# Kernel tuning notes

Measured on AMD Instinct MI355X. Metric: run time of the kernel, lower is better.

## Reference

```python
import jax, jax.numpy as jnp
import numpy as np

B, D, H, K, N = 1024, 768, 8, 10, 50000
LN_EPS = 1e-5


def _ln(x, g, b):
    m = x.mean(-1, keepdims=True)
    v = ((x - m) ** 2).mean(-1, keepdims=True)
    return (x - m) * jax.lax.rsqrt(v + LN_EPS) * g + b


def _normalize(x):
    n = jnp.sqrt(jnp.sum(x * x, -1, keepdims=True))
    return x / jnp.maximum(n, 1e-12)


def _mha(q, k, v, in_w, in_b, out_w, out_b, h=H):
    # torch nn.MultiheadAttention (batch_first, eval): packed in_proj then out_proj
    d = q.shape[-1]
    dh = d // h
    wq, wk, wv = jnp.split(in_w, 3, axis=0)
    bq, bk, bv = jnp.split(in_b, 3, axis=0)
    def proj(x, w, b):
        bsz, s, _ = x.shape
        return (x @ w.T + b).reshape(bsz, s, h, dh)
    qh, kh, vh = proj(q, wq, bq), proj(k, wk, bk), proj(v, wv, bv)
    att = jnp.einsum('bqhd,bkhd->bhqk', qh, kh) * (1.0 / np.sqrt(dh))
    att = jax.nn.softmax(att, axis=-1)
    o = jnp.einsum('bhqk,bkhd->bqhd', att, vh).reshape(q.shape[0], q.shape[1], d)
    return o @ out_w.T + out_b


def setup_inputs() -> dict:
    key = jax.random.key(0)
    ks = iter(jax.random.split(key, 32))
    s = 0.05
    r = lambda shp, sc=s: jax.random.normal(next(ks), shp, jnp.float32) * sc
    return {
        'visual_feat': r((B, D), 1.0), 'text_feat': r((B, D), 1.0),
        'ans_emb': r((N, D), 1.0),
        'vqa_in_w': r((3 * D, D)), 'vqa_in_b': jnp.zeros((3 * D,)),
        'vqa_out_w': r((D, D)), 'vqa_out_b': jnp.zeros((D,)),
        'fproj_w': r((D, 2 * D)), 'fproj_b': jnp.zeros((D,)),
        'fln_g': jnp.ones((D,)), 'fln_b': jnp.zeros((D,)),
        'sim_w': r((D, D)), 'sim_b': jnp.zeros((D,)),
        'mha_in_w': r((5, 3 * D, D)), 'mha_in_b': jnp.zeros((5, 3 * D)),
        'mha_out_w': r((5, D, D)), 'mha_out_b': jnp.zeros((5, D)),
        'ffn_w1': r((4 * D, D)), 'ffn_b1': jnp.zeros((4 * D,)),
        'ffn_w2': r((D, 4 * D)), 'ffn_b2': jnp.zeros((D,)),
        'ln_g': jnp.ones((4, D)), 'ln_b': jnp.zeros((4, D)),
        'outp_w': r((D, D)), 'outp_b': jnp.zeros((D,)),
        'open_w1': r((D, D)), 'open_b1': jnp.zeros((D,)),
        'open_w2': r((N, D)), 'open_b2': jnp.zeros((N,)),
    }


def reference(visual_feat, text_feat, ans_emb, vqa_in_w, vqa_in_b, vqa_out_w,
              vqa_out_b, fproj_w, fproj_b, fln_g, fln_b, sim_w, sim_b,
              mha_in_w, mha_in_b, mha_out_w, mha_out_b, ffn_w1, ffn_b1,
              ffn_w2, ffn_b2, ln_g, ln_b, outp_w, outp_b, open_w1, open_b1,
              open_w2, open_b2):
    gelu = lambda x: jax.nn.gelu(x, approximate=False)
    vis = visual_feat[:, None, :]   # [B,1,D]
    txt = text_feat[:, None, :]

    # --- SemanticAnswerDistillation ---
    attn_q = _mha(txt, vis, vis, vqa_in_w, vqa_in_b, vqa_out_w, vqa_out_b)[:, 0]
    fused = jnp.concatenate([visual_feat, attn_q], -1) @ fproj_w.T + fproj_b
    fused = gelu(_ln(fused, fln_g, fln_b))
    fused_proj = fused @ sim_w.T + sim_b
    sim = _normalize(fused_proj) @ _normalize(ans_emb).T   # [B,N] cosine sim
    topk_scores, topk_idx = jax.lax.top_k(sim, K)
    topk_emb = ans_emb[topk_idx]                           # [B,K,D] gather

    # --- CrossModalFusion --- (MHA order: vs, ts, v2t, t2v, ans)
    m = lambda i, q, k, v: _mha(q, k, v, mha_in_w[i], mha_in_b[i], mha_out_w[i], mha_out_b[i])
    v1 = _ln(vis + m(0, vis, vis, vis), ln_g[0], ln_b[0])
    t1 = _ln(txt + m(1, txt, txt, txt), ln_g[1], ln_b[1])
    fz = _ln(m(2, v1, t1, t1) + m(3, t1, v1, v1), ln_g[2], ln_b[2])
    ag = m(4, fz, topk_emb, topk_emb)
    fz = _ln(fz + ag, ln_g[3], ln_b[3])
    fz = fz + (gelu(fz @ ffn_w1.T + ffn_b1) @ ffn_w2.T + ffn_b2)
    out = fz[:, 0] @ outp_w.T + outp_b                     # [B,D]

    # --- open head ---
    open_logits = gelu(out @ open_w1.T + open_b1) @ open_w2.T + open_b2
    return open_logits
```

## Files before the change

### kernel.cpp

```cpp
#include <hip/hip_runtime.h>
#include <hip/hip_bf16.h>

#define D_  768
#define B_  1024
#define N_  50000
#define K_  10
#define CH2_ 12500
#define NCH2_ 4
#define CM2_ 16
#define KPT_ 49

__device__ __forceinline__ float gelu_f(float x){ return 0.5f*x*(1.0f+erff(x*0.70710678118654752f)); }
__device__ __forceinline__ double gelu_d(double x){ return 0.5*x*(1.0+erf(x*0.707106781186547524400844362105)); }

__device__ __forceinline__ float block_sum(float v, float* sm){
  #pragma unroll
  for (int o=32;o>0;o>>=1) v += __shfl_xor(v,o);
  __syncthreads();
  if ((threadIdx.x&63)==0) sm[threadIdx.x>>6]=v;
  __syncthreads();
  return (sm[0]+sm[1])+(sm[2]+sm[3]);
}
__device__ __forceinline__ double block_sum64(double v, double* sm){
  #pragma unroll
  for (int o=32;o>0;o>>=1) v += __shfl_xor(v,o);
  __syncthreads();
  if ((threadIdx.x&63)==0) sm[threadIdx.x>>6]=v;
  __syncthreads();
  return (sm[0]+sm[1])+(sm[2]+sm[3]);
}

template<int ASRC, int EPI>
__global__ __launch_bounds__(256)
void dgemm_k(const void* __restrict__ Ap, const float* __restrict__ Wp, size_t woff,
             const float* __restrict__ biasp, size_t boff, double* __restrict__ Cp,
             int M, int N, int Kd, int ldc)
{
  __shared__ double As[16][64];
  __shared__ double Bs[16][64];
  const int t  = threadIdx.x;
  const int tx = t & 15, ty = t >> 4;
  const int row0 = blockIdx.y << 6, col0 = blockIdx.x << 6;
  const int lr = t >> 2, lk = (t & 3) << 2;
  const int ar = row0 + lr;
  const int wn = col0 + lr;
  const float* Wf = Wp + woff;
  double acc[4][4] = {};
  for (int k0 = 0; k0 < Kd; k0 += 16) {
    double av[4], wv[4];
    if (ar < M) {
      if (ASRC==0){
        const double* a = (const double*)Ap + (size_t)ar*Kd + k0 + lk;
        av[0]=a[0]; av[1]=a[1]; av[2]=a[2]; av[3]=a[3];
      } else {
        float4 v = *(const float4*)((const float*)Ap + (size_t)ar*Kd + k0 + lk);
        av[0]=(double)v.x; av[1]=(double)v.y; av[2]=(double)v.z; av[3]=(double)v.w;
      }
    } else { av[0]=av[1]=av[2]=av[3]=0.0; }
    if (wn < N) {
      float4 v = *(const float4*)(Wf + (size_t)wn*Kd + k0 + lk);
      wv[0]=(double)v.x; wv[1]=(double)v.y; wv[2]=(double)v.z; wv[3]=(double)v.w;
    } else { wv[0]=wv[1]=wv[2]=wv[3]=0.0; }
    #pragma unroll
    for (int u=0;u<4;++u){ As[lk+u][lr]=av[u]; Bs[lk+u][lr]=wv[u]; }
    __syncthreads();
    #pragma unroll
    for (int kk=0;kk<16;++kk){
      double aa[4], bb[4];
      #pragma unroll
      for (int u=0;u<4;++u){ aa[u]=As[kk][(ty<<2)+u]; bb[u]=Bs[kk][(tx<<2)+u]; }
      #pragma unroll
      for (int i=0;i<4;++i)
        #pragma unroll
        for (int j=0;j<4;++j)
          acc[i][j] = fma(aa[i], bb[j], acc[i][j]);
    }
    __syncthreads();
  }
  #pragma unroll
  for (int i=0;i<4;++i){
    int r=row0+(ty<<2)+i; if (r>=M) continue;
    #pragma unroll
    for (int j=0;j<4;++j){
      int n=col0+(tx<<2)+j; if (n>=N) continue;
      double v=acc[i][j];
      if (EPI) v += (double)(biasp+boff)[n];
      Cp[(size_t)r*ldc+n]=v;
    }
  }
}

__global__ __launch_bounds__(256)
void ln64_k(const double* __restrict__ x0, const float* __restrict__ g,
            const float* __restrict__ b, double* __restrict__ y)
{
  __shared__ double sm[4];
  size_t base = (size_t)blockIdx.x * D_;
  double xv[3]; double s=0.0;
  #pragma unroll
  for (int i=0;i<3;++i){ int c=threadIdx.x+(i<<8); xv[i]=x0[base+c]; s+=xv[i]; }
  s = block_sum64(s, sm);
  double m = s*(1.0/768.0);
  double vs=0.0;
  #pragma unroll
  for (int i=0;i<3;++i){ double d=xv[i]-m; vs+=d*d; }
  vs = block_sum64(vs, sm);
  double inv = 1.0/sqrt(vs*(1.0/768.0)+1e-5);
  #pragma unroll
  for (int i=0;i<3;++i){
    int c=threadIdx.x+(i<<8);
    double o=(xv[i]-m)*inv*(double)g[c]+(double)b[c];
    y[base+c]=gelu_d(o);
  }
}

template<int SRC>
__global__ __launch_bounds__(256)
void rnorm64w_k(const void* __restrict__ x, double* __restrict__ invn, int M)
{
  int gw = (blockIdx.x*256 + threadIdx.x) >> 6;
  int lane = threadIdx.x & 63;
  if (gw >= M) return;
  size_t base = (size_t)gw * D_;
  double s = 0.0;
  #pragma unroll
  for (int k=0;k<12;++k){
    double v = (SRC==1) ? (double)((const float*)x)[base+lane+(k<<6)]
                        : ((const double*)x)[base+lane+(k<<6)];
    s = fma(v,v,s);
  }
  #pragma unroll
  for (int o=32;o>0;o>>=1) s += __shfl_xor(s,o);
  if (lane==0) invn[gw] = 1.0/fmax(sqrt(s),1e-12);
}

__global__ void d2f_k(const double* __restrict__ src, float* __restrict__ dst, int n)
{ int i=blockIdx.x*256+threadIdx.x; if (i<n) dst[i]=(float)src[i]; }

__global__ void prep64_k(const float* __restrict__ vis, double* __restrict__ fusedin)
{
  int i = blockIdx.x*256+threadIdx.x;
  if (i >= B_*D_) return;
  int r=i/D_, c=i-r*D_;
  fusedin[(size_t)r*(2*D_)+c]=(double)vis[i];
}

template<int EPI, int SCALE>
__global__ __launch_bounds__(256)
void gemm128_k(const float* __restrict__ Ap, const float* __restrict__ Wp,
               const float* __restrict__ biasp, float* __restrict__ Cp,
               const float* __restrict__ inva, const float* __restrict__ invw,
               int M, int N, int Kd, int ldc)
{
  __shared__ __align__(16) float As[16][128];
  __shared__ __align__(16) float Bs[16][128];
  const int t = threadIdx.x;
  const int tx = t & 15, ty = t >> 4;
  const int row0 = blockIdx.y << 7, col0 = blockIdx.x << 7;
  const int lr = t >> 1, lk8 = (t & 1) << 3;
  const int arow = row0 + lr;
  const int wrow = col0 + lr;
  float acc[8][8] = {};
  for (int k0 = 0; k0 < Kd; k0 += 16){
    float4 a0 = *(const float4*)(Ap + (size_t)arow*Kd + k0 + lk8);
    float4 a1 = *(const float4*)(Ap + (size_t)arow*Kd + k0 + lk8 + 4);
    float4 b0 = {0,0,0,0}, b1 = {0,0,0,0};
    if (wrow < N){
      b0 = *(const float4*)(Wp + (size_t)wrow*Kd + k0 + lk8);
      b1 = *(const float4*)(Wp + (size_t)wrow*Kd + k0 + lk8 + 4);
    }
    As[lk8+0][lr]=a0.x; As[lk8+1][lr]=a0.y; As[lk8+2][lr]=a0.z; As[lk8+3][lr]=a0.w;
    As[lk8+4][lr]=a1.x; As[lk8+5][lr]=a1.y; As[lk8+6][lr]=a1.z; As[lk8+7][lr]=a1.w;
    Bs[lk8+0][lr]=b0.x; Bs[lk8+1][lr]=b0.y; Bs[lk8+2][lr]=b0.z; Bs[lk8+3][lr]=b0.w;
    Bs[lk8+4][lr]=b1.x; Bs[lk8+5][lr]=b1.y; Bs[lk8+6][lr]=b1.z; Bs[lk8+7][lr]=b1.w;
    __syncthreads();
    #pragma unroll
    for (int kk=0; kk<16; ++kk){
      float4 aL = *(const float4*)&As[kk][ty<<2];
      float4 aH = *(const float4*)&As[kk][64 + (ty<<2)];
      float4 bL = *(const float4*)&Bs[kk][tx<<2];
      float4 bH = *(const float4*)&Bs[kk][64 + (tx<<2)];
      float av[8] = {aL.x,aL.y,aL.z,aL.w, aH.x,aH.y,aH.z,aH.w};
      float bv[8] = {bL.x,bL.y,bL.z,bL.w, bH.x,bH.y,bH.z,bH.w};
      #pragma unroll
      for (int i=0;i<8;++i)
        #pragma unroll
        for (int j=0;j<8;++j)
          acc[i][j] = fmaf(av[i], bv[j], acc[i][j]);
    }
    __syncthreads();
  }
  #pragma unroll
  for (int i=0;i<8;++i){
    int r = row0 + ((i<4) ? ((ty<<2)+i) : (64 + (ty<<2) + i - 4));
    float ia = SCALE ? inva[r] : 1.f;
    #pragma unroll
    for (int jh=0;jh<2;++jh){
      int cbase = col0 + ((jh==0) ? (tx<<2) : (64 + (tx<<2)));
      #pragma unroll
      for (int j=0;j<4;++j){
        int c = cbase + j;
        if (c >= N) continue;
        float v = acc[i][jh*4+j];
        if (EPI) v += biasp[c];
        if (SCALE) v = v * ia * invw[c];
        Cp[(size_t)r*ldc + c] = v;
      }
    }
  }
}

template<int ATY, int EPI, int SCALE>
__global__ __launch_bounds__(256)
void gemm_k(const float* __restrict__ Ap, const int* __restrict__ ridx,
            const float* __restrict__ Wp, size_t woff,
            const float* __restrict__ biasp, size_t boff, float* __restrict__ Cp,
            const float* __restrict__ inva32, const float* __restrict__ invw32,
            int M, int N, int Kd, int ldc)
{
  __shared__ __align__(16) float As[16][64];
  __shared__ __align__(16) float Bs[16][64];
  const int t  = threadIdx.x;
  const int tx = t & 15, ty = t >> 4;
  const int row0 = blockIdx.y << 6, col0 = blockIdx.x << 6;
  const int lr = t >> 2, lk = (t & 3) << 2;
  const int ar = row0 + lr;
  const int wn = col0 + lr;
  const float* Wf = Wp + woff;
  float acc[4][4] = {};
  int arow = ar;
  if (ATY==3 && ar < M){
    arow = ridx[ar];
    if ((unsigned)arow >= (unsigned)N_) arow = 0;
  }
  for (int k0 = 0; k0 < Kd; k0 += 16) {
    float av[4], wv[4];
    if (ar < M) {
      float4 v = *(const float4*)(Ap + (size_t)arow*Kd + k0 + lk);
      av[0]=v.x; av[1]=v.y; av[2]=v.z; av[3]=v.w;
    } else { av[0]=av[1]=av[2]=av[3]=0.f; }
    if (wn < N) {
      float4 v = *(const float4*)(Wf + (size_t)wn*Kd + k0 + lk);
      wv[0]=v.x; wv[1]=v.y; wv[2]=v.z; wv[3]=v.w;
    } else { wv[0]=wv[1]=wv[2]=wv[3]=0.f; }
    #pragma unroll
    for (int u=0;u<4;++u){ As[lk+u][lr]=av[u]; Bs[lk+u][lr]=wv[u]; }
    __syncthreads();
    #pragma unroll
    for (int kk=0;kk<16;++kk){
      float4 a4 = *(const float4*)&As[kk][ty<<2];
      float4 b4 = *(const float4*)&Bs[kk][tx<<2];
      float aa[4]={a4.x,a4.y,a4.z,a4.w};
      float bb[4]={b4.x,b4.y,b4.z,b4.w};
      #pragma unroll
      for (int i=0;i<4;++i)
        #pragma unroll
        for (int j=0;j<4;++j)
          acc[i][j] = fmaf(aa[i], bb[j], acc[i][j]);
    }
    __syncthreads();
  }
  float bv[4];
  #pragma unroll
  for (int j=0;j<4;++j){
    int n=col0+(tx<<2)+j;
    bv[j] = (EPI>=1 && n<N) ? (biasp+boff)[n] : 0.f;
  }
  #pragma unroll
  for (int i=0;i<4;++i){
    int r=row0+(ty<<2)+i; if (r>=M) continue;
    float ia = (SCALE && r<M) ? inva32[r] : 1.f;
    #pragma unroll
    for (int j=0;j<4;++j){
      int n=col0+(tx<<2)+j; if (n>=N) continue;
      float v=acc[i][j]+bv[j];
      if (EPI==2) v=gelu_f(v);
      if (SCALE) v = v * ia * invw32[n];
      Cp[(size_t)r*ldc+n]=v;
    }
  }
}

template<int RES>
__global__ __launch_bounds__(256)
void ln_k(const float* __restrict__ x0, const float* __restrict__ resf,
          const float* __restrict__ resb,
          const float* __restrict__ g, const float* __restrict__ b, size_t gboff,
          float* __restrict__ y)
{
  __shared__ float sm[4];
  size_t base = (size_t)blockIdx.x * D_;
  float xv[3]; float s=0.f;
  #pragma unroll
  for (int i=0;i<3;++i){
    int c=threadIdx.x+(i<<8);
    float tv=x0[base+c];
    if (RES==1) tv+=resf[base+c];
    if (RES==2) tv+=resb[base+c];
    xv[i]=tv; s+=tv;
  }
  s = block_sum(s, sm);
  float m = s*(1.0f/768.0f);
  float vs=0.f;
  #pragma unroll
  for (int i=0;i<3;++i){ float d=xv[i]-m; vs+=d*d; }
  vs = block_sum(vs, sm);
  float inv = rsqrtf(vs*(1.0f/768.0f)+1e-5f);
  #pragma unroll
  for (int i=0;i<3;++i){
    int c=threadIdx.x+(i<<8);
    y[base+c]=(xv[i]-m)*inv*(g+gboff)[c]+(b+gboff)[c];
  }
}

__global__ void add_k(const float* __restrict__ a, const float* __restrict__ b, float* __restrict__ c, int n)
{ int i=blockIdx.x*256+threadIdx.x; if (i<n) c[i]=a[i]+b[i]; }

__global__ __launch_bounds__(256)
void topk16_chunk_k(const float* __restrict__ simc, int* __restrict__ cand_id,
                    int off, int chunk, int cn, int ldc)
{
  __shared__ float rs[4];
  __shared__ int   ri[4];
  __shared__ float bs_s;
  __shared__ int   bi_s;
  int b = blockIdx.x, t = threadIdx.x;
  const float* rowp = simc + (size_t)b*ldc;
  float v[KPT_];
  #pragma unroll
  for (int k=0;k<KPT_;++k){
    int j = t + (k<<8);
    v[k] = (j < cn) ? rowp[j] : -1e30f;
  }
  float ps = 1e30f; int pi = -1;
  for (int round=0; round<CM2_; ++round){
    float ms = -1e30f; int mi = 0x7fffffff;
    #pragma unroll
    for (int k=0;k<KPT_;++k){
      int j = t + (k<<8);
      float s = v[k];
      bool elig = (s < ps) || (s == ps && j > pi);
      if (elig && (s > ms || (s == ms && j < mi))){ ms = s; mi = j; }
    }
    #pragma unroll
    for (int o=32;o>0;o>>=1){
      float os = __shfl_xor(ms, o); int oi = __shfl_xor(mi, o);
      if (os > ms || (os == ms && oi < mi)){ ms = os; mi = oi; }
    }
    if ((t&63)==0){ rs[t>>6]=ms; ri[t>>6]=mi; }
    __syncthreads();
    if (t==0){
      float gs=rs[0]; int gi=ri[0];
      #pragma unroll
      for (int w=1;w<4;++w) if (rs[w]>gs || (rs[w]==gs && ri[w]<gi)){ gs=rs[w]; gi=ri[w]; }
      bs_s=gs; bi_s=gi;
      cand_id[((size_t)b*NCH2_+chunk)*CM2_+round] = (gi==0x7fffffff) ? 0x7fffffff : off+gi;
    }
    __syncthreads();
    ps = bs_s; pi = bi_s;
  }
}

__global__ __launch_bounds__(256)
void rescore_k(const double* __restrict__ fproj64, const float* __restrict__ ans,
               const int* __restrict__ cand_id,
               const double* __restrict__ inv_fp64, const double* __restrict__ inv_an64,
               int* __restrict__ run_id)
{
  __shared__ double q[D_];
  __shared__ double sc_s[NCH2_*CM2_];
  __shared__ int    id_s[NCH2_*CM2_];
  int b = blockIdx.x, t = threadIdx.x;
  int wave = t>>6, lane = t&63;
  for (int i=t;i<D_;i+=256) q[i]=fproj64[(size_t)b*D_+i];
  __syncthreads();
  for (int c = wave; c < NCH2_*CM2_; c += 4){
    int j = cand_id[(size_t)b*NCH2_*CM2_ + c];
    bool ok = ((unsigned)j < (unsigned)N_);
    double acc = 0.0;
    if (ok){
      const float* ar = ans + (size_t)j*D_;
      #pragma unroll
      for (int k=0;k<12;++k){
        int d = lane + (k<<6);
        acc = fma(q[d], (double)ar[d], acc);
      }
    }
    #pragma unroll
    for (int o=32;o>0;o>>=1) acc += __shfl_xor(acc, o);
    if (lane==0){
      sc_s[c] = ok ? acc*inv_fp64[b]*inv_an64[j] : -1e300;
      id_s[c] = ok ? j : 0x7fffffff;
    }
  }
  __syncthreads();
  if (t==0){
    double gs[10]; int gi[10];
    #pragma unroll
    for (int k=0;k<10;++k){ gs[k]=-1e300; gi[k]=0x7fffffff; }
    for (int i=0;i<NCH2_*CM2_;++i){
      double s=sc_s[i]; int id=id_s[i];
      bool better9 = (s>gs[9]) || (s==gs[9] && id<gi[9]);
      if (!better9) continue;
      int q9=9;
      while (q9>0 && (gs[q9-1]<s || (gs[q9-1]==s && gi[q9-1]>id))){
        gs[q9]=gs[q9-1]; gi[q9]=gi[q9-1]; --q9;
      }
      gs[q9]=s; gi[q9]=id;
    }
    #pragma unroll
    for (int k=0;k<10;++k) run_id[b*10+k]=gi[k];
  }
}

__global__ __launch_bounds__(64)
void attn2_k(const float* __restrict__ qh, const float* __restrict__ kvh,
             float* __restrict__ o)
{
  int idx = blockIdx.x*64 + threadIdx.x;
  if (idx >= B_*8) return;
  int b = idx >> 3, h = idx & 7;
  const float* q = qh + (size_t)b*D_ + h*96;
  float p[10];
  float mx = -1e30f;
  for (int j=0;j<10;++j){
    const float* kr = kvh + ((size_t)(b*10+j))*1536 + h*96;
    float acc=0.f;
    for (int d=0;d<96;++d) acc = fmaf(q[d], kr[d], acc);
    p[j] = acc * 0.10206207261596575f;
    mx = fmaxf(mx, p[j]);
  }
  float sum=0.f;
  for (int j=0;j<10;++j){ p[j]=expf(p[j]-mx); sum+=p[j]; }
  float inv=1.0f/sum;
  for (int d=0;d<96;++d){
    float acc=0.f;
    for (int j=0;j<10;++j) acc = fmaf(p[j]*inv, kvh[((size_t)(b*10+j))*1536 + 768 + h*96 + d], acc);
    o[(size_t)b*D_ + h*96 + d] = acc;
  }
}

extern "C" void kernel_launch(void* const* d_in, const int* in_sizes, int n_in,
                              void* d_out, int out_size, void* d_ws, size_t ws_size,
                              hipStream_t stream)
{
  const float* vis      = (const float*)d_in[0];
  const float* txt      = (const float*)d_in[1];
  const float* ans      = (const float*)d_in[2];
  const float* vqa_in_w = (const float*)d_in[3];
  const float* vqa_in_b = (const float*)d_in[4];
  const float* vqa_out_w= (const float*)d_in[5];
  const float* vqa_out_b= (const float*)d_in[6];
  const float* fproj_w  = (const float*)d_in[7];
  const float* fproj_b  = (const float*)d_in[8];
  const float* fln_g    = (const float*)d_in[9];
  const float* fln_b    = (const float*)d_in[10];
  const float* sim_w    = (const float*)d_in[11];
  const float* sim_b    = (const float*)d_in[12];
  const float* m_in_w   = (const float*)d_in[13];
  const float* m_in_b   = (const float*)d_in[14];
  const float* m_out_w  = (const float*)d_in[15];
  const float* m_out_b  = (const float*)d_in[16];
  const float* ffn_w1   = (const float*)d_in[17];
  const float* ffn_b1   = (const float*)d_in[18];
  const float* ffn_w2   = (const float*)d_in[19];
  const float* ffn_b2   = (const float*)d_in[20];
  const float* ln_g     = (const float*)d_in[21];
  const float* ln_b     = (const float*)d_in[22];
  const float* outp_w   = (const float*)d_in[23];
  const float* outp_b   = (const float*)d_in[24];
  const float* open_w1  = (const float*)d_in[25];
  const float* open_b1  = (const float*)d_in[26];
  const float* open_w2  = (const float*)d_in[27];
  const float* open_b2  = (const float*)d_in[28];
  (void)n_in; (void)out_size;

  if (in_sizes[0]!=B_*D_) return;
  if (in_sizes[1]!=B_*D_) return;
  if (in_sizes[2]!=N_*D_) return;
  if (in_sizes[3]!=3*D_*D_) return;
  if (in_sizes[4]!=3*D_) return;
  if (in_sizes[5]!=D_*D_) return;
  if (in_sizes[7]!=D_*2*D_) return;
  if (in_sizes[9]!=D_) return;
  if (in_sizes[13]!=5*3*D_*D_) return;
  if (in_sizes[14]!=5*3*D_) return;
  if (in_sizes[15]!=5*D_*D_) return;
  if (in_sizes[17]!=4*D_*D_) return;
  if (in_sizes[19]!=4*D_*D_) return;
  if (in_sizes[21]!=4*D_) return;
  if (in_sizes[23]!=D_*D_) return;
  if (in_sizes[25]!=D_*D_) return;
  if (in_sizes[27]!=N_*D_) return;

  const size_t MBc = (size_t)1<<20;
  if (ws_size < 84*MBc) return;
  char* base = (char*)d_ws;
  double* fusedin64 = (double*)(base + 0);
  double* attn_v64  = (double*)(base + 12*MBc);
  double* ta64      = (double*)(base + 12*MBc);
  double* fused64   = (double*)(base + 18*MBc);
  double* fproj64   = (double*)(base + 60*MBc);
  float*  fproj32   = (float*) (base + 66*MBc);
  float*  sim_ch    = (float*) (base + 0);
  double* inv_an64  = (double*)(base + 69*MBc);
  double* inv_fp64  = (double*)(base + 70*MBc);
  float*  inv_an32  = (float*) (base + 71*MBc);
  float*  inv_fp32  = (float*) (base + 72*MBc);
  int*    cand_id   = (int*)   (base + 73*MBc);
  int*    run_id    = (int*)   (base + 78*MBc);
  float* kvh  = (float*)(base + 0);
  float* h1   = (float*)(base + 0);
  float* ta   = (float*)(base + 60*MBc);
  float* tb   = (float*)(base + 63*MBc);
  float* tc   = (float*)(base + 66*MBc);
  float* fz0  = (float*)(base + 66*MBc);
  float* td   = (float*)(base + 69*MBc);
  float* fz   = (float*)(base + 69*MBc);
  float* v1   = (float*)(base + 72*MBc);
  float* o4   = (float*)(base + 72*MBc);
  float* outv = (float*)(base + 72*MBc);
  float* t1   = (float*)(base + 75*MBc);
  float* qh   = (float*)(base + 75*MBc);
  float* g1   = (float*)(base + 75*MBc);

  dim3 blk(256);
  auto gg = [](int M,int N){ return dim3((unsigned)((N+63)/64),(unsigned)((M+63)/64)); };
  auto g128 = [](int M,int N){ return dim3((unsigned)((N+127)/128),(unsigned)(M/128)); };
  auto ng = [](int M,int N){ return dim3((unsigned)(((size_t)M*N+255)/256)); };
  const size_t IW = (size_t)2304*768, OW = (size_t)768*768;
  const size_t VOFF = (size_t)1536*768, KOFF = (size_t)768*768;
  const int* NORIDX = nullptr;
  const float* NOS = nullptr;

  prep64_k<<<ng(B_,D_), blk, 0, stream>>>(vis, fusedin64);
  dgemm_k<1,1><<<gg(B_,D_), blk, 0, stream>>>(vis, vqa_in_w, VOFF, vqa_in_b, 1536, attn_v64, B_, D_, D_, D_);
  dgemm_k<0,1><<<gg(B_,D_), blk, 0, stream>>>(attn_v64, vqa_out_w, 0, vqa_out_b, 0, fusedin64+D_, B_, D_, D_, 2*D_);
  dgemm_k<0,1><<<gg(B_,D_), blk, 0, stream>>>(fusedin64, fproj_w, 0, fproj_b, 0, ta64, B_, D_, 2*D_, D_);
  ln64_k<<<B_, blk, 0, stream>>>(ta64, fln_g, fln_b, fused64);
  dgemm_k<0,1><<<gg(B_,D_), blk, 0, stream>>>(fused64, sim_w, 0, sim_b, 0, fproj64, B_, D_, D_, D_);
  rnorm64w_k<1><<<(N_*64+255)/256, blk, 0, stream>>>(ans, inv_an64, N_);
  rnorm64w_k<0><<<(B_*64+255)/256, blk, 0, stream>>>(fproj64, inv_fp64, B_);
  d2f_k<<<(N_+255)/256, blk, 0, stream>>>(inv_an64, inv_an32, N_);
  d2f_k<<<(B_+255)/256, blk, 0, stream>>>(inv_fp64, inv_fp32, B_);
  d2f_k<<<(B_*D_+255)/256, blk, 0, stream>>>(fproj64, fproj32, B_*D_);
  for (int c=0;c<NCH2_;++c){
    gemm128_k<0,1><<<g128(B_,CH2_), blk, 0, stream>>>(fproj32, ans + (size_t)c*CH2_*D_, nullptr, sim_ch, inv_fp32, inv_an32 + c*CH2_, B_, CH2_, D_, CH2_);
    topk16_chunk_k<<<B_, blk, 0, stream>>>(sim_ch, cand_id, c*CH2_, c, CH2_, CH2_);
  }
  rescore_k<<<B_, blk, 0, stream>>>(fproj64, ans, cand_id, inv_fp64, inv_an64, run_id);

  gemm_k<2,1,0><<<gg(B_,D_), blk, 0, stream>>>(vis, NORIDX, m_in_w, 0*IW+VOFF, m_in_b, 0*2304+1536, ta, NOS, NOS, B_, D_, D_, D_);
  gemm_k<0,1,0><<<gg(B_,D_), blk, 0, stream>>>(ta, NORIDX, m_out_w, 0*OW, m_out_b, 0*768, tb, NOS, NOS, B_, D_, D_, D_);
  ln_k<2><<<B_, blk, 0, stream>>>(tb, nullptr, vis, ln_g, ln_b, 0*D_, v1);
  gemm_k<2,1,0><<<gg(B_,D_), blk, 0, stream>>>(txt, NORIDX, m_in_w, 1*IW+VOFF, m_in_b, 1*2304+1536, ta, NOS, NOS, B_, D_, D_, D_);
  gemm_k<0,1,0><<<gg(B_,D_), blk, 0, stream>>>(ta, NORIDX, m_out_w, 1*OW, m_out_b, 1*768, tb, NOS, NOS, B_, D_, D_, D_);
  ln_k<2><<<B_, blk, 0, stream>>>(tb, nullptr, txt, ln_g, ln_b, 1*D_, t1);
  gemm_k<0,1,0><<<gg(B_,D_), blk, 0, stream>>>(t1, NORIDX, m_in_w, 2*IW+VOFF, m_in_b, 2*2304+1536, ta, NOS, NOS, B_, D_, D_, D_);
  gemm_k<0,1,0><<<gg(B_,D_), blk, 0, stream>>>(ta, NORIDX, m_out_w, 2*OW, m_out_b, 2*768, tb, NOS, NOS, B_, D_, D_, D_);
  gemm_k<0,1,0><<<gg(B_,D_), blk, 0, stream>>>(v1, NORIDX, m_in_w, 3*IW+VOFF, m_in_b, 3*2304+1536, tc, NOS, NOS, B_, D_, D_, D_);
  gemm_k<0,1,0><<<gg(B_,D_), blk, 0, stream>>>(tc, NORIDX, m_out_w, 3*OW, m_out_b, 3*768, td, NOS, NOS, B_, D_, D_, D_);
  ln_k<1><<<B_, blk, 0, stream>>>(tb, td, nullptr, ln_g, ln_b, 2*D_, fz0);
  gemm_k<0,1,0><<<gg(B_,D_), blk, 0, stream>>>(fz0, NORIDX, m_in_w, 4*IW, m_in_b, 4*2304, qh, NOS, NOS, B_, D_, D_, D_);
  gemm_k<3,1,0><<<gg(B_*K_,2*D_), blk, 0, stream>>>(ans, run_id, m_in_w, 4*IW+KOFF, m_in_b, 4*2304+768, kvh, NOS, NOS, B_*K_, 2*D_, D_, 2*D_);
  attn2_k<<<(B_*8+63)/64, dim3(64), 0, stream>>>(qh, kvh, o4);
  gemm_k<0,1,0><<<gg(B_,D_), blk, 0, stream>>>(o4, NORIDX, m_out_w, 4*OW, m_out_b, 4*768, ta, NOS, NOS, B_, D_, D_, D_);
  ln_k<1><<<B_, blk, 0, stream>>>(fz0, ta, nullptr, ln_g, ln_b, 3*D_, fz);
  gemm_k<0,2,0><<<gg(B_,4*D_), blk, 0, stream>>>(fz, NORIDX, ffn_w1, 0, ffn_b1, 0, h1, NOS, NOS, B_, 4*D_, D_, 4*D_);
  gemm_k<0,1,0><<<gg(B_,D_), blk, 0, stream>>>(h1, NORIDX, ffn_w2, 0, ffn_b2, 0, tb, NOS, NOS, B_, D_, 4*D_, D_);
  add_k<<<ng(B_,D_), blk, 0, stream>>>(fz, tb, ta, B_*D_);
  gemm_k<0,1,0><<<gg(B_,D_), blk, 0, stream>>>(ta, NORIDX, outp_w, 0, outp_b, 0, outv, NOS, NOS, B_, D_, D_, D_);
  gemm_k<0,2,0><<<gg(B_,D_), blk, 0, stream>>>(outv, NORIDX, open_w1, 0, open_b1, 0, g1, NOS, NOS, B_, D_, D_, D_);
  gemm128_k<1,0><<<g128(B_,N_), blk, 0, stream>>>(g1, open_w2, open_b2, (float*)d_out, NOS, NOS, B_, N_, D_, N_);
}
```

Measured before the change: 4.463 ms.

## Prefetch next K-tile in gemm128, batch paired MHA GEMMs, gather KV via gemm128

The 128x128 SGEMM now loads the next K-slice of A and W into registers while the current slice is being computed from shared memory. This hides global-load latency in the two large 1024x50000 GEMMs. Paired independent attention projections (vs/ts, v2t/t2v) are launched together in a new batched 64x64 tiled kernel indexed by blockIdx.z, which halves the launch count and fills more of the GPU. The gathered top-k K/V projection moves to the larger-tile gemm128 kernel through a new row-gather template path. The cost is higher register pressure in gemm128 and a simpler, unpipelined small-tile kernel for the batched projections.

```diff
diff --git a/kernel.cpp b/kernel.cpp
--- a/kernel.cpp
+++ b/kernel.cpp
@@ -145,9 +145,10 @@
   fusedin[(size_t)r*(2*D_)+c]=(double)vis[i];
 }
 
-template<int EPI, int SCALE>
-__global__ __launch_bounds__(256)
-void gemm128_k(const float* __restrict__ Ap, const float* __restrict__ Wp,
+template<int EPI, int SCALE, int GATHER>
+__global__ __launch_bounds__(256)
+void gemm128_k(const float* __restrict__ Ap, const int* __restrict__ ridx,
+               const float* __restrict__ Wp,
                const float* __restrict__ biasp, float* __restrict__ Cp,
                const float* __restrict__ inva, const float* __restrict__ invw,
                int M, int N, int Kd, int ldc)
@@ -158,22 +159,33 @@
   const int tx = t & 15, ty = t >> 4;
   const int row0 = blockIdx.y << 7, col0 = blockIdx.x << 7;
   const int lr = t >> 1, lk8 = (t & 1) << 3;
-  const int arow = row0 + lr;
+  int arow = row0 + lr;
+  if (GATHER){ int gidx = ridx[arow]; arow = ((unsigned)gidx < (unsigned)N_) ? gidx : 0; }
   const int wrow = col0 + lr;
+  const bool wok = (wrow < N);
+  const float* aptr = Ap + (size_t)arow*Kd + lk8;
+  const float* wptr = Wp + (size_t)(wok ? wrow : 0)*Kd + lk8;
   float acc[8][8] = {};
-  for (int k0 = 0; k0 < Kd; k0 += 16){
-    float4 a0 = *(const float4*)(Ap + (size_t)arow*Kd + k0 + lk8);
-    float4 a1 = *(const float4*)(Ap + (size_t)arow*Kd + k0 + lk8 + 4);
-    float4 b0 = {0,0,0,0}, b1 = {0,0,0,0};
-    if (wrow < N){
-      b0 = *(const float4*)(Wp + (size_t)wrow*Kd + k0 + lk8);
-      b1 = *(const float4*)(Wp + (size_t)wrow*Kd + k0 + lk8 + 4);
-    }
+  float4 z; z.x=z.y=z.z=z.w=0.f;
+  float4 a0 = *(const float4*)(aptr);
+  float4 a1 = *(const float4*)(aptr+4);
+  float4 b0 = wok ? *(const float4*)(wptr)   : z;
+  float4 b1 = wok ? *(const float4*)(wptr+4) : z;
+  const int nt = Kd >> 4;
+  for (int it=0; it<nt; ++it){
     As[lk8+0][lr]=a0.x; As[lk8+1][lr]=a0.y; As[lk8+2][lr]=a0.z; As[lk8+3][lr]=a0.w;
     As[lk8+4][lr]=a1.x; As[lk8+5][lr]=a1.y; As[lk8+6][lr]=a1.z; As[lk8+7][lr]=a1.w;
     Bs[lk8+0][lr]=b0.x; Bs[lk8+1][lr]=b0.y; Bs[lk8+2][lr]=b0.z; Bs[lk8+3][lr]=b0.w;
     Bs[lk8+4][lr]=b1.x; Bs[lk8+5][lr]=b1.y; Bs[lk8+6][lr]=b1.z; Bs[lk8+7][lr]=b1.w;
     __syncthreads();
+    if (it+1 < nt){
+      const float* ap = aptr + ((it+1)<<4);
+      a0 = *(const float4*)(ap); a1 = *(const float4*)(ap+4);
+      if (wok){
+        const float* wp = wptr + ((it+1)<<4);
+        b0 = *(const float4*)(wp); b1 = *(const float4*)(wp+4);
+      }
+    }
     #pragma unroll
     for (int kk=0; kk<16; ++kk){
       float4 aL = *(const float4*)&As[kk][ty<<2];
@@ -277,6 +289,54 @@
       if (EPI==2) v=gelu_f(v);
       if (SCALE) v = v * ia * invw32[n];
       Cp[(size_t)r*ldc+n]=v;
+    }
+  }
+}
+
+__global__ __launch_bounds__(256)
+void gemm2_k(const float* __restrict__ A0, const float* __restrict__ A1,
+             const float* __restrict__ W, size_t w0, size_t w1,
+             const float* __restrict__ bias, size_t bo0, size_t bo1,
+             float* __restrict__ C0, float* __restrict__ C1)
+{
+  const float* Ap = blockIdx.z ? A1 : A0;
+  const float* Wf = W + (blockIdx.z ? w1 : w0);
+  const float* bp = bias + (blockIdx.z ? bo1 : bo0);
+  float* Cp = blockIdx.z ? C1 : C0;
+  __shared__ __align__(16) float As[16][64];
+  __shared__ __align__(16) float Bs[16][64];
+  const int t  = threadIdx.x;
+  const int tx = t & 15, ty = t >> 4;
+  const int row0 = blockIdx.y << 6, col0 = blockIdx.x << 6;
+  const int lr = t >> 2, lk = (t & 3) << 2;
+  float acc[4][4] = {};
+  for (int k0 = 0; k0 < D_; k0 += 16) {
+    float4 va = *(const float4*)(Ap + (size_t)(row0+lr)*D_ + k0 + lk);
+    float4 vw = *(const float4*)(Wf + (size_t)(col0+lr)*D_ + k0 + lk);
+    As[lk+0][lr]=va.x; As[lk+1][lr]=va.y; As[lk+2][lr]=va.z; As[lk+3][lr]=va.w;
+    Bs[lk+0][lr]=vw.x; Bs[lk+1][lr]=vw.y; Bs[lk+2][lr]=vw.z; Bs[lk+3][lr]=vw.w;
+    __syncthreads();
+    #pragma unroll
+    for (int kk=0;kk<16;++kk){
+      float4 a4 = *(const float4*)&As[kk][ty<<2];
+      float4 b4 = *(const float4*)&Bs[kk][tx<<2];
+      float aa[4]={a4.x,a4.y,a4.z,a4.w};
+      float bb[4]={b4.x,b4.y,b4.z,b4.w};
+      #pragma unroll
+      for (int i=0;i<4;++i)
+        #pragma unroll
+        for (int j=0;j<4;++j)
+          acc[i][j] = fmaf(aa[i], bb[j], acc[i][j]);
+    }
+    __syncthreads();
+  }
+  #pragma unroll
+  for (int i=0;i<4;++i){
+    int r=row0+(ty<<2)+i;
+    #pragma unroll
+    for (int j=0;j<4;++j){
+      int n=col0+(tx<<2)+j;
+      Cp[(size_t)r*D_+n]=acc[i][j]+bp[n];
     }
   }
 }
@@ -545,24 +605,20 @@
   d2f_k<<<(B_+255)/256, blk, 0, stream>>>(inv_fp64, inv_fp32, B_);
   d2f_k<<<(B_*D_+255)/256, blk, 0, stream>>>(fproj64, fproj32, B_*D_);
   for (int c=0;c<NCH2_;++c){
-    gemm128_k<0,1><<<g128(B_,CH2_), blk, 0, stream>>>(fproj32, ans + (size_t)c*CH2_*D_, nullptr, sim_ch, inv_fp32, inv_an32 + c*CH2_, B_, CH2_, D_, CH2_);
+    gemm128_k<0,1,0><<<g128(B_,CH2_), blk, 0, stream>>>(fproj32, NORIDX, ans + (size_t)c*CH2_*D_, nullptr, sim_ch, inv_fp32, inv_an32 + c*CH2_, B_, CH2_, D_, CH2_);
     topk16_chunk_k<<<B_, blk, 0, stream>>>(sim_ch, cand_id, c*CH2_, c, CH2_, CH2_);
   }
   rescore_k<<<B_, blk, 0, stream>>>(fproj64, ans, cand_id, inv_fp64, inv_an64, run_id);
 
-  gemm_k<2,1,0><<<gg(B_,D_), blk, 0, stream>>>(vis, NORIDX, m_in_w, 0*IW+VOFF, m_in_b, 0*2304+1536, ta, NOS, NOS, B_, D_, D_, D_);
-  gemm_k<0,1,0><<<gg(B_,D_), blk, 0, stream>>>(ta, NORIDX, m_out_w, 0*OW, m_out_b, 0*768, tb, NOS, NOS, B_, D_, D_, D_);
-  ln_k<2><<<B_, blk, 0, stream>>>(tb, nullptr, vis, ln_g, ln_b, 0*D_, v1);
-  gemm_k<2,1,0><<<gg(B_,D_), blk, 0, stream>>>(txt, NORIDX, m_in_w, 1*IW+VOFF, m_in_b, 1*2304+1536, ta, NOS, NOS, B_, D_, D_, D_);
-  gemm_k<0,1,0><<<gg(B_,D_), blk, 0, stream>>>(ta, NORIDX, m_out_w, 1*OW, m_out_b, 1*768, tb, NOS, NOS, B_, D_, D_, D_);
-  ln_k<2><<<B_, blk, 0, stream>>>(tb, nullptr, txt, ln_g, ln_b, 1*D_, t1);
-  gemm_k<0,1,0><<<gg(B_,D_), blk, 0, stream>>>(t1, NORIDX, m_in_w, 2*IW+VOFF, m_in_b, 2*2304+1536, ta, NOS, NOS, B_, D_, D_, D_);
-  gemm_k<0,1,0><<<gg(B_,D_), blk, 0, stream>>>(ta, NORIDX, m_out_w, 2*OW, m_out_b, 2*768, tb, NOS, NOS, B_, D_, D_, D_);
-  gemm_k<0,1,0><<<gg(B_,D_), blk, 0, stream>>>(v1, NORIDX, m_in_w, 3*IW+VOFF, m_in_b, 3*2304+1536, tc, NOS, NOS, B_, D_, D_, D_);
-  gemm_k<0,1,0><<<gg(B_,D_), blk, 0, stream>>>(tc, NORIDX, m_out_w, 3*OW, m_out_b, 3*768, td, NOS, NOS, B_, D_, D_, D_);
-  ln_k<1><<<B_, blk, 0, stream>>>(tb, td, nullptr, ln_g, ln_b, 2*D_, fz0);
+  gemm2_k<<<dim3(12,16,2), blk, 0, stream>>>(vis, txt, m_in_w, 0*IW+VOFF, 1*IW+VOFF, m_in_b, 0*2304+1536, 1*2304+1536, ta, tb);
+  gemm2_k<<<dim3(12,16,2), blk, 0, stream>>>(ta, tb, m_out_w, 0*OW, 1*OW, m_out_b, 0*768, 1*768, tc, td);
+  ln_k<2><<<B_, blk, 0, stream>>>(tc, nullptr, vis, ln_g, ln_b, 0*D_, v1);
+  ln_k<2><<<B_, blk, 0, stream>>>(td, nullptr, txt, ln_g, ln_b, 1*D_, t1);
+  gemm2_k<<<dim3(12,16,2), blk, 0, stream>>>(t1, v1, m_in_w, 2*IW+VOFF, 3*IW+VOFF, m_in_b, 2*2304+1536, 3*2304+1536, ta, tb);
+  gemm2_k<<<dim3(12,16,2), blk, 0, stream>>>(ta, tb, m_out_w, 2*OW, 3*OW, m_out_b, 2*768, 3*768, tc, td);
+  ln_k<1><<<B_, blk, 0, stream>>>(tc, td, nullptr, ln_g, ln_b, 2*D_, fz0);
   gemm_k<0,1,0><<<gg(B_,D_), blk, 0, stream>>>(fz0, NORIDX, m_in_w, 4*IW, m_in_b, 4*2304, qh, NOS, NOS, B_, D_, D_, D_);
-  gemm_k<3,1,0><<<gg(B_*K_,2*D_), blk, 0, stream>>>(ans, run_id, m_in_w, 4*IW+KOFF, m_in_b, 4*2304+768, kvh, NOS, NOS, B_*K_, 2*D_, D_, 2*D_);
+  gemm128_k<1,0,1><<<g128(B_*K_, 2*D_), blk, 0, stream>>>(ans, run_id, m_in_w + 4*IW + KOFF, m_in_b + 4*2304 + 768, kvh, NOS, NOS, B_*K_, 2*D_, D_, 2*D_);
   attn2_k<<<(B_*8+63)/64, dim3(64), 0, stream>>>(qh, kvh, o4);
   gemm_k<0,1,0><<<gg(B_,D_), blk, 0, stream>>>(o4, NORIDX, m_out_w, 4*OW, m_out_b, 4*768, ta, NOS, NOS, B_, D_, D_, D_);
   ln_k<1><<<B_, blk, 0, stream>>>(fz0, ta, nullptr, ln_g, ln_b, 3*D_, fz);
@@ -571,5 +627,5 @@
   add_k<<<ng(B_,D_), blk, 0, stream>>>(fz, tb, ta, B_*D_);
   gemm_k<0,1,0><<<gg(B_,D_), blk, 0, stream>>>(ta, NORIDX, outp_w, 0, outp_b, 0, outv, NOS, NOS, B_, D_, D_, D_);
   gemm_k<0,2,0><<<gg(B_,D_), blk, 0, stream>>>(outv, NORIDX, open_w1, 0, open_b1, 0, g1, NOS, NOS, B_, D_, D_, D_);
-  gemm128_k<1,0><<<g128(B_,N_), blk, 0, stream>>>(g1, open_w2, open_b2, (float*)d_out, NOS, NOS, B_, N_, D_, N_);
-}
+  gemm128_k<1,0,0><<<g128(B_,N_), blk, 0, stream>>>(g1, NORIDX, open_w2, open_b2, (float*)d_out, NOS, NOS, B_, N_, D_, N_);
+}
```

Measured after the change: 4.196 ms. 6.0% less time.
